# Kernel optimization log

Measured on AMD Instinct MI355X. Metric: run time of the kernel, lower is better.

The kernel has to match this reference:

```python
import jax, jax.numpy as jnp
import numpy as np

B, S, I, H = 16, 2048, 1024, 1024

def setup_inputs() -> dict:
    key = jax.random.key(0)
    ks = jax.random.split(key, 6)
    scale_ih = 1.0 / np.sqrt(I)
    scale_hh = 1.0 / np.sqrt(H)
    return {
        "x": jax.random.normal(ks[0], (B, S, I), dtype=jnp.float32),
        "hx": jax.random.normal(ks[1], (B, H), dtype=jnp.float32),
        "W_ih": jax.random.normal(ks[2], (H, I), dtype=jnp.float32) * scale_ih,
        "W_hh": jax.random.normal(ks[3], (H, H), dtype=jnp.float32) * scale_hh,
        "b_ih": jax.random.normal(ks[4], (H,), dtype=jnp.float32) * scale_ih,
        "b_hh": jax.random.normal(ks[5], (H,), dtype=jnp.float32) * scale_hh,
    }

def reference(x, hx, W_ih, W_hh, b_ih, b_hh):
    # Faithful to RecurrentCellWrapper: the Python loop passes the SAME
    # initial hx to the cell at every timestep (hx is never updated),
    # so all steps are independent and fully vectorizable.
    # cell: h' = tanh(x_t @ W_ih^T + b_ih + hx @ W_hh^T + b_hh)
    h_term = hx @ W_hh.T + b_hh + b_ih            # [B, H], shared across steps
    x_term = jnp.einsum('bsi,hi->bsh', x, W_ih)   # [B, S, H]
    out = jnp.tanh(x_term + h_term[:, None, :])   # [B, S, H]
    # batch_first=True: output already [batch, seq, hidden]
    return out
```

## Files before the change

kernel.cpp:

```cpp
#include <hip/hip_runtime.h>
#include <stdint.h>


#define M_TOT 32768
#define N_TOT 1024
#define K_TOT 1024

typedef short short8 __attribute__((ext_vector_type(8)));
typedef float f32x4  __attribute__((ext_vector_type(4)));

#define WS_WBF_OFF 0
#define WS_HT_OFF  2097152

__device__ __forceinline__ unsigned int pack2_bf16_rne(float lo, float hi) {
    unsigned int a = __float_as_uint(lo);
    unsigned int b = __float_as_uint(hi);
    a = (a + 0x7fffu + ((a >> 16) & 1u)) >> 16;
    b = (b + 0x7fffu + ((b >> 16) & 1u)) & 0xffff0000u;
    return a | b;
}

__device__ __forceinline__ float fast_tanh(float z) {
    float e = __expf(2.0f * z);
    return 1.0f - 2.0f / (e + 1.0f);
}

__global__ void prep_kernel(const float* __restrict__ hx,
                            const float* __restrict__ whh,
                            const float* __restrict__ bih,
                            const float* __restrict__ bhh,
                            const float* __restrict__ wih,
                            unsigned short* __restrict__ wbf,
                            float* __restrict__ ht) {
    int bid = blockIdx.x;
    if (bid < 4096) {
        int lane = threadIdx.x & 63;
        int w    = threadIdx.x >> 6;
        int wg   = bid * 4 + w;
        int b = wg >> 10, h = wg & 1023;
        const float* hr = hx  + (long long)b * 1024;
        const float* wr = whh + (long long)h * 1024;
        float s = 0.f;
#pragma unroll
        for (int p = 0; p < 4; ++p) {
            int idx = p * 256 + lane * 4;
            float4 a = *(const float4*)(hr + idx);
            float4 c = *(const float4*)(wr + idx);
            s += a.x * c.x + a.y * c.y + a.z * c.z + a.w * c.w;
        }
#pragma unroll
        for (int d = 32; d > 0; d >>= 1) s += __shfl_down(s, d, 64);
        if (lane == 0) ht[wg] = s + bih[h] + bhh[h];
    } else {
        long long base = ((long long)(bid - 4096) * 256 + threadIdx.x) * 8;
        float4 a = *(const float4*)(wih + base);
        float4 b = *(const float4*)(wih + base + 4);
        uint4 o;
        o.x = pack2_bf16_rne(a.x, a.y);
        o.y = pack2_bf16_rne(a.z, a.w);
        o.z = pack2_bf16_rne(b.x, b.y);
        o.w = pack2_bf16_rne(b.z, b.w);
        *(uint4*)(wbf + base) = o;
    }
}

#define GLDS16(gp, lp) \
    __builtin_amdgcn_global_load_lds((const __attribute__((address_space(1))) void*)(gp), \
                                     (__attribute__((address_space(3))) void*)(lp), 16, 0, 0)

__global__ __launch_bounds__(256) void gemm_tanh_kernel(
    const float* __restrict__ X,
    const unsigned short* __restrict__ Bm,
    const float* __restrict__ ht,
    float* __restrict__ out)
{
    __shared__ __align__(16) char lds[16384];

    const int tid = threadIdx.x;
    const int w = tid >> 6, l = tid & 63;

    const int bid = blockIdx.x;
    const int x = bid & 7;
    const int tile_n = (bid >> 3) & 7;
    const int g = bid >> 6;
    const int tile_m = x * 32 + g;
    const int m0 = tile_m << 7, n0 = tile_n << 7;

    const int r0 = (w * 2 + 0) * 16 + (l >> 2);
    const int r1 = (w * 2 + 1) * 16 + (l >> 2);
    const int slot = l & 3;
    const int qg0 = (slot - (r0 >> 1)) & 3;
    const int qg1 = (slot - (r1 >> 1)) & 3;
    const unsigned short* gB0 = Bm + (long long)(n0 + r0) * K_TOT + qg0 * 8;
    const unsigned short* gB1 = Bm + (long long)(n0 + r1) * K_TOT + qg1 * 8;
    char* ldsB0 = lds + 8192 + (w * 2 + 0) * 1024;
    char* ldsB1 = lds + 8192 + (w * 2 + 1) * 1024;

    const int rowA0 = tid >> 2;
    const int rowA1 = rowA0 + 64;
    const int sA = tid & 3;
    const int qgA0 = (sA - (rowA0 >> 1)) & 3;
    const int qgA1 = (sA - (rowA1 >> 1)) & 3;
    const float* gAf0 = X + (long long)(m0 + rowA0) * K_TOT + qgA0 * 8;
    const float* gAf1 = X + (long long)(m0 + rowA1) * K_TOT + qgA1 * 8;
    const int ldsAoff0 = rowA0 * 64 + sA * 16;
    const int ldsAoff1 = rowA1 * 64 + sA * 16;

    const int wm = w & 1, wn = w >> 1;
    const int lm = l & 15, q = l >> 4;
    int offA[4], offB[4];
#pragma unroll
    for (int t = 0; t < 4; ++t) {
        int rr = wm * 64 + t * 16 + lm;
        offA[t] = rr * 64 + (((q + (rr >> 1)) & 3) << 4);
        int nn = wn * 64 + t * 16 + lm;
        offB[t] = 8192 + nn * 64 + (((q + (nn >> 1)) & 3) << 4);
    }

    f32x4 acc[4][4];
#pragma unroll
    for (int i = 0; i < 4; ++i)
#pragma unroll
        for (int j = 0; j < 4; ++j)
            acc[i][j] = (f32x4){0.f, 0.f, 0.f, 0.f};

    for (int k0 = 0; k0 < K_TOT; k0 += 32) {
        GLDS16(gB0 + k0, ldsB0);
        GLDS16(gB1 + k0, ldsB1);
        float4 a00 = *(const float4*)(gAf0 + k0);
        float4 a01 = *(const float4*)(gAf0 + k0 + 4);
        float4 a10 = *(const float4*)(gAf1 + k0);
        float4 a11 = *(const float4*)(gAf1 + k0 + 4);
        uint4 w0, w1;
        w0.x = pack2_bf16_rne(a00.x, a00.y);
        w0.y = pack2_bf16_rne(a00.z, a00.w);
        w0.z = pack2_bf16_rne(a01.x, a01.y);
        w0.w = pack2_bf16_rne(a01.z, a01.w);
        w1.x = pack2_bf16_rne(a10.x, a10.y);
        w1.y = pack2_bf16_rne(a10.z, a10.w);
        w1.z = pack2_bf16_rne(a11.x, a11.y);
        w1.w = pack2_bf16_rne(a11.z, a11.w);
        *(uint4*)(lds + ldsAoff0) = w0;
        *(uint4*)(lds + ldsAoff1) = w1;
        __syncthreads();

        short8 af[4], bf[4];
#pragma unroll
        for (int t = 0; t < 4; ++t) {
            af[t] = *(const short8*)(lds + offA[t]);
            bf[t] = *(const short8*)(lds + offB[t]);
        }
#pragma unroll
        for (int mt = 0; mt < 4; ++mt)
#pragma unroll
            for (int nt = 0; nt < 4; ++nt)
                acc[mt][nt] = __builtin_amdgcn_mfma_f32_16x16x32_bf16(
                    af[mt], bf[nt], acc[mt][nt], 0, 0, 0);
        __syncthreads();
    }

    const int b = tile_m >> 4;
    float htv[4];
#pragma unroll
    for (int nt = 0; nt < 4; ++nt)
        htv[nt] = ht[b * 1024 + n0 + wn * 64 + nt * 16 + lm];

#pragma unroll
    for (int mt = 0; mt < 4; ++mt) {
#pragma unroll
        for (int nt = 0; nt < 4; ++nt) {
            int n = n0 + wn * 64 + nt * 16 + lm;
#pragma unroll
            for (int r = 0; r < 4; ++r) {
                int m = m0 + wm * 64 + mt * 16 + q * 4 + r;
                float z = acc[mt][nt][r] + htv[nt];
                out[(long long)m * N_TOT + n] = fast_tanh(z);
            }
        }
    }
}

extern "C" void kernel_launch(void* const* d_in, const int* in_sizes, int n_in,
                              void* d_out, int out_size, void* d_ws, size_t ws_size,
                              hipStream_t stream) {
    const float* x    = (const float*)d_in[0];
    const float* hx   = (const float*)d_in[1];
    const float* wih  = (const float*)d_in[2];
    const float* whh  = (const float*)d_in[3];
    const float* bih  = (const float*)d_in[4];
    const float* bhh  = (const float*)d_in[5];
    float* out = (float*)d_out;

    unsigned short* wbf = (unsigned short*)((char*)d_ws + WS_WBF_OFF);
    float*          htp = (float*)((char*)d_ws + WS_HT_OFF);

    prep_kernel<<<4608, 256, 0, stream>>>(hx, whh, bih, bhh, wih, wbf, htp);
    gemm_tanh_kernel<<<2048, 256, 0, stream>>>(x, wbf, htp, out);
}
```

Before: 361.9 us.

## Load fp32 A tiles directly to LDS and convert to bf16 at fragment read

The GEMM kernel now streams fp32 X tiles into LDS with async global_load_lds instead of loading through registers, packing to bf16 and storing. Conversion to bf16 moves to the point where MFMA fragments are read from LDS, using a new 8-slot swizzle for the 128-byte fp32 rows. This removes the register round-trip and the VALU packing before the barrier, but doubles LDS footprint for A and does the packing per fragment read. The prep kernel is also restructured so one block computes all 16 batch dot products for a hidden unit, reusing each W_hh row.

```diff
diff --git a/kernel.cpp b/kernel.cpp
--- a/kernel.cpp
+++ b/kernel.cpp
@@ -33,26 +33,32 @@
                             unsigned short* __restrict__ wbf,
                             float* __restrict__ ht) {
     int bid = blockIdx.x;
-    if (bid < 4096) {
-        int lane = threadIdx.x & 63;
-        int w    = threadIdx.x >> 6;
-        int wg   = bid * 4 + w;
-        int b = wg >> 10, h = wg & 1023;
-        const float* hr = hx  + (long long)b * 1024;
-        const float* wr = whh + (long long)h * 1024;
-        float s = 0.f;
-#pragma unroll
-        for (int p = 0; p < 4; ++p) {
-            int idx = p * 256 + lane * 4;
-            float4 a = *(const float4*)(hr + idx);
-            float4 c = *(const float4*)(wr + idx);
-            s += a.x * c.x + a.y * c.y + a.z * c.z + a.w * c.w;
-        }
-#pragma unroll
-        for (int d = 32; d > 0; d >>= 1) s += __shfl_down(s, d, 64);
-        if (lane == 0) ht[wg] = s + bih[h] + bhh[h];
+    if (bid < 1024) {
+        __shared__ float red[16][256];
+        const int h = bid;
+        const int t = threadIdx.x;
+        float4 wv = *(const float4*)(whh + (long long)h * 1024 + t * 4);
+        float p[16];
+#pragma unroll
+        for (int b = 0; b < 16; ++b) {
+            float4 xv = *(const float4*)(hx + (long long)b * 1024 + t * 4);
+            p[b] = wv.x * xv.x + wv.y * xv.y + wv.z * xv.z + wv.w * xv.w;
+        }
+#pragma unroll
+        for (int b = 0; b < 16; ++b) red[b][t] = p[b];
+        __syncthreads();
+        const int w = t >> 6, lane = t & 63;
+#pragma unroll
+        for (int bb = 0; bb < 4; ++bb) {
+            int b = w * 4 + bb;
+            float4 v = *(const float4*)(&red[b][lane * 4]);
+            float s = v.x + v.y + v.z + v.w;
+#pragma unroll
+            for (int d = 32; d > 0; d >>= 1) s += __shfl_down(s, d, 64);
+            if (lane == 0) ht[b * 1024 + h] = s + bih[h] + bhh[h];
+        }
     } else {
-        long long base = ((long long)(bid - 4096) * 256 + threadIdx.x) * 8;
+        long long base = ((long long)(bid - 1024) * 256 + threadIdx.x) * 8;
         float4 a = *(const float4*)(wih + base);
         float4 b = *(const float4*)(wih + base + 4);
         uint4 o;
@@ -74,47 +80,52 @@
     const float* __restrict__ ht,
     float* __restrict__ out)
 {
-    __shared__ __align__(16) char lds[16384];
+    __shared__ __align__(16) char lds[24576];
 
     const int tid = threadIdx.x;
     const int w = tid >> 6, l = tid & 63;
 
     const int bid = blockIdx.x;
-    const int x = bid & 7;
+    const int xcd = bid & 7;
     const int tile_n = (bid >> 3) & 7;
     const int g = bid >> 6;
-    const int tile_m = x * 32 + g;
+    const int tile_m = xcd * 32 + g;
     const int m0 = tile_m << 7, n0 = tile_n << 7;
+
+    const int arow = l >> 3;
+    const int aslot = l & 7;
+    const int aq = (aslot - arow) & 7;
+    const float* gA[4];
+    char* ldsA[4];
+#pragma unroll
+    for (int j = 0; j < 4; ++j) {
+        int rbase = w * 32 + j * 8;
+        gA[j] = X + (long long)(m0 + rbase + arow) * K_TOT + aq * 4;
+        ldsA[j] = lds + rbase * 128;
+    }
 
     const int r0 = (w * 2 + 0) * 16 + (l >> 2);
     const int r1 = (w * 2 + 1) * 16 + (l >> 2);
-    const int slot = l & 3;
-    const int qg0 = (slot - (r0 >> 1)) & 3;
-    const int qg1 = (slot - (r1 >> 1)) & 3;
+    const int bslot = l & 3;
+    const int qg0 = (bslot - (r0 >> 1)) & 3;
+    const int qg1 = (bslot - (r1 >> 1)) & 3;
     const unsigned short* gB0 = Bm + (long long)(n0 + r0) * K_TOT + qg0 * 8;
     const unsigned short* gB1 = Bm + (long long)(n0 + r1) * K_TOT + qg1 * 8;
-    char* ldsB0 = lds + 8192 + (w * 2 + 0) * 1024;
-    char* ldsB1 = lds + 8192 + (w * 2 + 1) * 1024;
-
-    const int rowA0 = tid >> 2;
-    const int rowA1 = rowA0 + 64;
-    const int sA = tid & 3;
-    const int qgA0 = (sA - (rowA0 >> 1)) & 3;
-    const int qgA1 = (sA - (rowA1 >> 1)) & 3;
-    const float* gAf0 = X + (long long)(m0 + rowA0) * K_TOT + qgA0 * 8;
-    const float* gAf1 = X + (long long)(m0 + rowA1) * K_TOT + qgA1 * 8;
-    const int ldsAoff0 = rowA0 * 64 + sA * 16;
-    const int ldsAoff1 = rowA1 * 64 + sA * 16;
+    char* ldsB0 = lds + 16384 + (w * 2 + 0) * 1024;
+    char* ldsB1 = lds + 16384 + (w * 2 + 1) * 1024;
 
     const int wm = w & 1, wn = w >> 1;
     const int lm = l & 15, q = l >> 4;
-    int offA[4], offB[4];
+    int offA0[4], offA1[4], offB[4];
 #pragma unroll
     for (int t = 0; t < 4; ++t) {
         int rr = wm * 64 + t * 16 + lm;
-        offA[t] = rr * 64 + (((q + (rr >> 1)) & 3) << 4);
+        int p0 = (2 * q + 0 + (rr & 7)) & 7;
+        int p1 = (2 * q + 1 + (rr & 7)) & 7;
+        offA0[t] = rr * 128 + p0 * 16;
+        offA1[t] = rr * 128 + p1 * 16;
         int nn = wn * 64 + t * 16 + lm;
-        offB[t] = 8192 + nn * 64 + (((q + (nn >> 1)) & 3) << 4);
+        offB[t] = 16384 + nn * 64 + (((q + (nn >> 1)) & 3) << 4);
     }
 
     f32x4 acc[4][4];
@@ -125,29 +136,23 @@
             acc[i][j] = (f32x4){0.f, 0.f, 0.f, 0.f};
 
     for (int k0 = 0; k0 < K_TOT; k0 += 32) {
+#pragma unroll
+        for (int j = 0; j < 4; ++j) GLDS16(gA[j] + k0, ldsA[j]);
         GLDS16(gB0 + k0, ldsB0);
         GLDS16(gB1 + k0, ldsB1);
-        float4 a00 = *(const float4*)(gAf0 + k0);
-        float4 a01 = *(const float4*)(gAf0 + k0 + 4);
-        float4 a10 = *(const float4*)(gAf1 + k0);
-        float4 a11 = *(const float4*)(gAf1 + k0 + 4);
-        uint4 w0, w1;
-        w0.x = pack2_bf16_rne(a00.x, a00.y);
-        w0.y = pack2_bf16_rne(a00.z, a00.w);
-        w0.z = pack2_bf16_rne(a01.x, a01.y);
-        w0.w = pack2_bf16_rne(a01.z, a01.w);
-        w1.x = pack2_bf16_rne(a10.x, a10.y);
-        w1.y = pack2_bf16_rne(a10.z, a10.w);
-        w1.z = pack2_bf16_rne(a11.x, a11.y);
-        w1.w = pack2_bf16_rne(a11.z, a11.w);
-        *(uint4*)(lds + ldsAoff0) = w0;
-        *(uint4*)(lds + ldsAoff1) = w1;
         __syncthreads();
 
         short8 af[4], bf[4];
 #pragma unroll
         for (int t = 0; t < 4; ++t) {
-            af[t] = *(const short8*)(lds + offA[t]);
+            float4 f0 = *(const float4*)(lds + offA0[t]);
+            float4 f1 = *(const float4*)(lds + offA1[t]);
+            uint4 p;
+            p.x = pack2_bf16_rne(f0.x, f0.y);
+            p.y = pack2_bf16_rne(f0.z, f0.w);
+            p.z = pack2_bf16_rne(f1.x, f1.y);
+            p.w = pack2_bf16_rne(f1.z, f1.w);
+            af[t] = *(short8*)&p;
             bf[t] = *(const short8*)(lds + offB[t]);
         }
 #pragma unroll
@@ -194,6 +199,6 @@
     unsigned short* wbf = (unsigned short*)((char*)d_ws + WS_WBF_OFF);
     float*          htp = (float*)((char*)d_ws + WS_HT_OFF);
 
-    prep_kernel<<<4608, 256, 0, stream>>>(hx, whh, bih, bhh, wih, wbf, htp);
+    prep_kernel<<<1536, 256, 0, stream>>>(hx, whh, bih, bhh, wih, wbf, htp);
     gemm_tanh_kernel<<<2048, 256, 0, stream>>>(x, wbf, htp, out);
 }
```

New measurement: 403.6 us. +11.5%, slower.
